# Kernel optimization log

Hardware: AMD Instinct MI355X
Metric: run time of the kernel (lower is better)

## Reference

```python
import jax, jax.numpy as jnp
import numpy as np

B, N, A = 32, 1024, 256          # batch, n_entities, n_agents
D_IN, D_H, H = 256, 256, 8       # input_dim, hidden_dim, n_heads
SCALE = 1.0 / np.sqrt(D_H)
EPS = 1e-12


def setup_inputs() -> dict:
    key = jax.random.key(0)
    ks = jax.random.split(key, 7)
    x = jax.random.normal(ks[0], (B, N, D_IN), dtype=jnp.float32)
    # binary visibility mask [batch, n_agents, n_entities]
    m = (jax.random.uniform(ks[1], (B, A, N)) > 0.5).astype(jnp.float32)
    # encoder Linear(input_dim, hidden_dim): weight [out,in], bias [out]
    W_enc = jax.random.normal(ks[2], (D_H, D_IN), dtype=jnp.float32) / np.sqrt(D_IN)
    b_enc = jnp.zeros((D_H,), dtype=jnp.float32)
    # per-head projection matrices stacked [H, D_H, D_H] (torch.randn init)
    WQ = jax.random.normal(ks[3], (H, D_H, D_H), dtype=jnp.float32)
    WK = jax.random.normal(ks[4], (H, D_H, D_H), dtype=jnp.float32)
    WV = jax.random.normal(ks[5], (H, D_H, D_H), dtype=jnp.float32)
    return {"x": x, "m": m, "W_enc": W_enc, "b_enc": b_enc, "WQ": WQ, "WK": WK, "WV": WV}


def reference(x, m, W_enc, b_enc, WQ, WK, WV):
    # encode: LeakyReLU then Linear
    h = jnp.einsum('bni,oi->bno', jax.nn.leaky_relu(x), W_enc) + b_enc  # [B,N,D_H]
    n_agents = m.shape[1]
    ha = h[:, :n_agents]                                   # [B,A,D_H]
    # per-head projections, heads vectorized
    Q = jnp.einsum('bad,hde->bhae', ha, WQ)                # [B,H,A,D_H]
    K = jnp.einsum('bnd,hde->bhne', h, WK)                 # [B,H,N,D_H]
    V = jnp.einsum('bnd,hde->bhne', h, WV)                 # [B,H,N,D_H]
    S = jnp.einsum('bhae,bhne->bhan', Q, K) * SCALE        # [B,H,A,N]
    P = jax.nn.softmax(S, axis=-1)
    P = P * m[:, None]                                     # post-softmax mask
    prob = P / (jnp.sum(P, axis=-1, keepdims=True) + EPS)  # renormalize
    z = jnp.einsum('bhan,bhne->bhae', prob, V)             # [B,H,A,D_H]
    return jnp.mean(z, axis=1)                             # [B,A,D_H]
```

## Files before the change

### kernel.cpp

```cpp
#include <hip/hip_runtime.h>
#include <math.h>

namespace {
constexpr int B_N  = 32;
constexpr int SEQ  = 1024;
constexpr int AG   = 256;
constexpr int D    = 256;
constexpr int NH   = 8;
constexpr float SCALE = 0.0625f;
constexpr float EPS   = 1e-12f;

constexpr size_t HHI_OFF  = 0;
constexpr size_t HLO_OFF  = 16777216;
constexpr size_t HT_OFF   = 33554432;
constexpr size_t MTHI_OFF = 50331648;
constexpr size_t MTLO_OFF = 51380224;
constexpr size_t MB_OFF   = 52428800;
constexpr size_t WVT_OFF  = 53477376;
constexpr size_t Z16_OFF  = 54525952;
}

typedef __attribute__((ext_vector_type(8))) short short8;
typedef __attribute__((ext_vector_type(4))) float floatx4;
#define MFMA_BF(A,B,C) __builtin_amdgcn_mfma_f32_16x16x32_bf16(A,B,C,0,0,0)

__device__ __forceinline__ unsigned short bf16_rtne(float f) {
    unsigned u = __float_as_uint(f);
    u += 0x7fffu + ((u >> 16) & 1u);
    return (unsigned short)(u >> 16);
}
__device__ __forceinline__ float bf16_tof(unsigned short h) {
    return __uint_as_float(((unsigned)h) << 16);
}
__device__ __forceinline__ void async16(void* lds, const void* g) {
    __builtin_amdgcn_global_load_lds(
        (const __attribute__((address_space(1))) unsigned int*)g,
        (__attribute__((address_space(3))) unsigned int*)lds,
        16, 0, 0);
}

__global__ __launch_bounds__(256) void enc_prep(
    const float* __restrict__ x, const float* __restrict__ W_enc,
    const float* __restrict__ b_enc,
    ushort* __restrict__ h_hi, ushort* __restrict__ h_lo,
    ushort* __restrict__ hT,
    const float* __restrict__ m, unsigned* __restrict__ mb,
    const float* __restrict__ WV, ushort* __restrict__ WVt,
    const float* __restrict__ WQ, const float* __restrict__ WK,
    ushort* __restrict__ Mt_hi, ushort* __restrict__ Mt_lo)
{
    __shared__ __align__(16) char slds[38912];
    const int t = threadIdx.x;
    const int v = blockIdx.x;

    if (v < 2048) {
        ushort (*Ah)[40] = (ushort(*)[40])(slds);
        ushort (*Al)[40] = (ushort(*)[40])(slds + 5120);
        ushort (*Bh)[40] = (ushort(*)[40])(slds + 10240);
        ushort (*Bl)[40] = (ushort(*)[40])(slds + 15360);
        ushort (*Th)[72] = (ushort(*)[72])(slds + 20480);
        ushort (*Tl)[72] = (ushort(*)[72])(slds + 29696);

        const int wv   = t >> 6;
        const int lane = t & 63;
        const int l15  = lane & 15;
        const int quad = lane >> 4;
        const int col0 = (v & 3) * 64;
        const int vy   = v >> 2;
        const int row0 = vy * 64;

        floatx4 acc[4];
#pragma unroll
        for (int i = 0; i < 4; ++i) acc[i] = (floatx4){0.f, 0.f, 0.f, 0.f};

        for (int k0 = 0; k0 < 256; k0 += 32) {
            __syncthreads();
            {
                const int r = t >> 2, s = (t & 3) * 8;
                float f[8];
                *(float4*)&f[0] = *(const float4*)(x + (size_t)(row0 + r) * 256 + k0 + s);
                *(float4*)&f[4] = *(const float4*)(x + (size_t)(row0 + r) * 256 + k0 + s + 4);
                short8 hi8, lo8;
#pragma unroll
                for (int e = 0; e < 8; ++e) {
                    float vv = f[e] > 0.f ? f[e] : 0.01f * f[e];
                    unsigned short hb = bf16_rtne(vv);
                    hi8[e] = (short)hb;
                    lo8[e] = (short)bf16_rtne(vv - bf16_tof(hb));
                }
                *(short8*)&Ah[r][s] = hi8;
                *(short8*)&Al[r][s] = lo8;
                *(float4*)&f[0] = *(const float4*)(W_enc + (size_t)(col0 + r) * 256 + k0 + s);
                *(float4*)&f[4] = *(const float4*)(W_enc + (size_t)(col0 + r) * 256 + k0 + s + 4);
#pragma unroll
                for (int e = 0; e < 8; ++e) {
                    unsigned short hb = bf16_rtne(f[e]);
                    hi8[e] = (short)hb;
                    lo8[e] = (short)bf16_rtne(f[e] - bf16_tof(hb));
                }
                *(short8*)&Bh[r][s] = hi8;
                *(short8*)&Bl[r][s] = lo8;
            }
            __syncthreads();

            short8 Af  = *(const short8*)&Ah[wv * 16 + l15][quad * 8];
            short8 Afl = *(const short8*)&Al[wv * 16 + l15][quad * 8];
#pragma unroll
            for (int et = 0; et < 4; ++et) {
                short8 Bf  = *(const short8*)&Bh[et * 16 + l15][quad * 8];
                short8 Bfl = *(const short8*)&Bl[et * 16 + l15][quad * 8];
                acc[et] = MFMA_BF(Af,  Bf,  acc[et]);
                acc[et] = MFMA_BF(Afl, Bf,  acc[et]);
                acc[et] = MFMA_BF(Af,  Bfl, acc[et]);
            }
        }

        __syncthreads();
#pragma unroll
        for (int et = 0; et < 4; ++et) {
            const int col = et * 16 + l15;
            const float bb = b_enc[col0 + col];
#pragma unroll
            for (int r = 0; r < 4; ++r) {
                const int row = wv * 16 + quad * 4 + r;
                const float vv = acc[et][r] + bb;
                const unsigned short hb = bf16_rtne(vv);
                Th[row][col] = hb;
                Tl[row][col] = bf16_rtne(vv - bf16_tof(hb));
            }
        }
        __syncthreads();
        {
            const int r = t >> 2, c0 = (t & 3) * 16;
            ushort* dh = h_hi + (size_t)(row0 + r) * 256 + col0 + c0;
            ushort* dl = h_lo + (size_t)(row0 + r) * 256 + col0 + c0;
            *(short8*)dh       = *(const short8*)&Th[r][c0];
            *(short8*)(dh + 8) = *(const short8*)&Th[r][c0 + 8];
            *(short8*)dl       = *(const short8*)&Tl[r][c0];
            *(short8*)(dl + 8) = *(const short8*)&Tl[r][c0 + 8];
        }
        {
            const int bq = vy >> 4;
            const int n0 = (vy & 15) * 64;
            const int dd = t >> 2, seg = (t & 3) * 16;
            ushort tmp[16];
#pragma unroll
            for (int j = 0; j < 16; ++j) tmp[j] = Th[seg + j][dd];
            ushort* dst = hT + ((size_t)(bq * 256 + col0 + dd)) * 1024 + n0 + seg;
            *(short8*)dst       = *(short8*)&tmp[0];
            *(short8*)(dst + 8) = *(short8*)&tmp[8];
        }
    } else if (v < 3072) {
        const int idx = (v - 2048) * 256 + t;
        const float4* src = (const float4*)(m + (size_t)idx * 32);
        unsigned wbits = 0;
#pragma unroll
        for (int i = 0; i < 8; ++i) {
            float4 vv = src[i];
            wbits |= (vv.x > 0.5f ? 1u : 0u) << (i * 4 + 0);
            wbits |= (vv.y > 0.5f ? 1u : 0u) << (i * 4 + 1);
            wbits |= (vv.z > 0.5f ? 1u : 0u) << (i * 4 + 2);
            wbits |= (vv.w > 0.5f ? 1u : 0u) << (i * 4 + 3);
        }
        mb[idx] = wbits;
    } else if (v < 3200) {
        float (*T)[68] = (float(*)[68])slds;
        const int v2 = v - 3072;
        const int d0 = (v2 & 3) * 64, e0 = ((v2 >> 2) & 3) * 64, h = v2 >> 4;
        {
            const int r = t >> 2, c = (t & 3) * 16;
            const float* src = WV + ((size_t)(h * 256 + d0 + r)) * 256 + e0 + c;
#pragma unroll
            for (int j = 0; j < 4; ++j)
                *(float4*)&T[r][c + j * 4] = *(const float4*)(src + j * 4);
        }
        __syncthreads();
        {
            const int ee = t >> 2, seg = (t & 3) * 16;
            ushort tmp[16];
#pragma unroll
            for (int j = 0; j < 16; ++j) tmp[j] = bf16_rtne(T[seg + j][ee]);
            ushort* dst = WVt + ((size_t)(h * 256 + e0 + ee)) * 256 + d0 + seg;
            *(short8*)dst       = *(short8*)&tmp[0];
            *(short8*)(dst + 8) = *(short8*)&tmp[8];
        }
    } else {
        float (*AsT)[68] = (float(*)[68])slds;
        float (*BsT)[68] = (float(*)[68])(slds + 8704);
        const int v3 = v - 3200;
        const int tx = t & 15, ty = t >> 4;
        const int col0 = (v3 & 3) * 64;
        const int row0 = ((v3 >> 2) & 3) * 64;
        const int hz   = v3 >> 4;
        const float* A  = WK + (size_t)hz * 256 * 256;
        const float* Bm = WQ + (size_t)hz * 256 * 256;
        ushort* Chi = Mt_hi + (size_t)hz * 256 * 256;
        ushort* Clo = Mt_lo + (size_t)hz * 256 * 256;

        float acc[4][4];
#pragma unroll
        for (int r = 0; r < 4; ++r)
#pragma unroll
            for (int c = 0; c < 4; ++c) acc[r][c] = 0.f;

        for (int k0 = 0; k0 < 256; k0 += 32) {
            __syncthreads();
#pragma unroll
            for (int ss = 0; ss < 2; ++ss) {
                int flat = t + 256 * ss;
                int rr = flat >> 3, k4 = flat & 7;
                float4 vv = *(const float4*)(A + (size_t)(row0 + rr) * 256 + k0 + k4 * 4);
                AsT[k4*4+0][rr] = vv.x; AsT[k4*4+1][rr] = vv.y;
                AsT[k4*4+2][rr] = vv.z; AsT[k4*4+3][rr] = vv.w;
                float4 wv = *(const float4*)(Bm + (size_t)(col0 + rr) * 256 + k0 + k4 * 4);
                BsT[k4*4+0][rr] = wv.x; BsT[k4*4+1][rr] = wv.y;
                BsT[k4*4+2][rr] = wv.z; BsT[k4*4+3][rr] = wv.w;
            }
            __syncthreads();
#pragma unroll 8
            for (int kk = 0; kk < 32; ++kk) {
                float4 a4 = *(const float4*)&AsT[kk][ty * 4];
                float4 b4 = *(const float4*)&BsT[kk][tx * 4];
                const float ar[4] = {a4.x, a4.y, a4.z, a4.w};
                const float bc[4] = {b4.x, b4.y, b4.z, b4.w};
#pragma unroll
                for (int r = 0; r < 4; ++r)
#pragma unroll
                    for (int c = 0; c < 4; ++c)
                        acc[r][c] = fmaf(ar[r], bc[c], acc[r][c]);
            }
        }
#pragma unroll
        for (int r = 0; r < 4; ++r) {
            const int row = row0 + ty * 4 + r;
            ushort hi4[4], lo4[4];
#pragma unroll
            for (int c = 0; c < 4; ++c) {
                float vv = acc[r][c];
                hi4[c] = bf16_rtne(vv);
                lo4[c] = bf16_rtne(vv - bf16_tof(hi4[c]));
            }
            *(ushort4*)(Chi + (size_t)row * 256 + col0 + tx * 4) =
                make_ushort4(hi4[0], hi4[1], hi4[2], hi4[3]);
            *(ushort4*)(Clo + (size_t)row * 256 + col0 + tx * 4) =
                make_ushort4(lo4[0], lo4[1], lo4[2], lo4[3]);
        }
    }
}

__global__ __launch_bounds__(512, 2) void attn_mfma(
    const ushort* __restrict__ h_hi, const ushort* __restrict__ h_lo,
    const ushort* __restrict__ hT,   const ushort* __restrict__ Mt_hi,
    const ushort* __restrict__ Mt_lo, const unsigned* __restrict__ mbits,
    ushort* __restrict__ zout)
{
    __shared__ __align__(16) char lds[118784];
    ushort* pP = (ushort*)(lds + 98304);
    ushort* pE = (ushort*)(lds + 108544);

    const int t    = threadIdx.x;
    const int wv   = t >> 6;
    const int lane = t & 63;
    const int l15  = lane & 15;
    const int quad = lane >> 4;
    const int f    = blockIdx.x;
    const int b    = (f & 7) + 8 * (f >> 7);
    const int mid  = (f >> 3) & 15;
    const int hh   = (mid >> 2) * 2 + (wv >> 2);
    const int a0   = (mid & 3) * 64;
    const int aw   = a0 + (wv & 3) * 16;

    const ushort* hbh = h_hi + (size_t)b * SEQ * D;
    const ushort* hbl = h_lo + (size_t)b * SEQ * D;
    const ushort* hTb = hT   + (size_t)b * D * SEQ;

    floatx4 qac[16];
#pragma unroll
    for (int i = 0; i < 16; ++i) qac[i] = (floatx4){0.f, 0.f, 0.f, 0.f};

    for (int kc = 0; kc < 4; ++kc) {
        short8 Ah[2], Al[2];
#pragma unroll
        for (int kt = 0; kt < 2; ++kt) {
            const size_t ao = ((size_t)b * SEQ + aw + l15) * D +
                              kc * 64 + kt * 32 + quad * 8;
            Ah[kt] = *(const short8*)(h_hi + ao);
            Al[kt] = *(const short8*)(h_lo + ao);
        }
#pragma unroll
        for (int nt2 = 0; nt2 < 16; ++nt2) {
#pragma unroll
            for (int kt = 0; kt < 2; ++kt) {
                const size_t mo = ((size_t)hh * D + nt2 * 16 + l15) * D +
                                  kc * 64 + kt * 32 + quad * 8;
                short8 Bh = *(const short8*)(Mt_hi + mo);
                short8 Bl = *(const short8*)(Mt_lo + mo);
                qac[nt2] = MFMA_BF(Ah[kt], Bh, qac[nt2]);
                qac[nt2] = MFMA_BF(Al[kt], Bh, qac[nt2]);
                qac[nt2] = MFMA_BF(Ah[kt], Bl, qac[nt2]);
            }
        }
    }

    short8 Qhi[8], Qlo[8];
    {
        float* qscr = (float*)lds;
        for (int c = 0; c < 4; ++c) {
#pragma unroll
            for (int j = 0; j < 4; ++j)
#pragma unroll
                for (int r = 0; r < 4; ++r)
                    qscr[(wv * 16 + quad * 4 + r) * 68 + j * 16 + l15] = qac[c * 4 + j][r];
#pragma unroll
            for (int kt = 0; kt < 2; ++kt) {
                const float* pr = &qscr[(wv * 16 + l15) * 68 + kt * 32 + quad * 8];
                float ftmp[8];
                *(float4*)&ftmp[0] = *(const float4*)pr;
                *(float4*)&ftmp[4] = *(const float4*)(pr + 4);
                short8 hi, lo;
#pragma unroll
                for (int e = 0; e < 8; ++e) {
                    unsigned short hb = bf16_rtne(ftmp[e]);
                    hi[e] = (short)hb;
                    lo[e] = (short)bf16_rtne(ftmp[e] - bf16_tof(hb));
                }
                Qhi[c * 2 + kt] = hi;
                Qlo[c * 2 + kt] = lo;
            }
        }
    }
    __syncthreads();

    auto issue_tile = [&](char* buf, int n0) {
        ushort* dh = (ushort*)buf;
        ushort* dl = (ushort*)(buf + 16384);
        ushort* dT = (ushort*)(buf + 32768);
#pragma unroll
        for (int i = 0; i < 2; ++i) {
            const int slot = wv * 128 + i * 64 + lane;
            const int row  = slot >> 5;
            const int p    = slot & 31;
            const int c    = p ^ (row & 7);
            const size_t go = (size_t)(n0 + row) * 256 + c * 8;
            const size_t lo_ = (size_t)(wv * 128 + i * 64) * 8;
            async16(dh + lo_, hbh + go);
            async16(dl + lo_, hbl + go);
        }
#pragma unroll
        for (int i = 0; i < 2; ++i) {
            const int slot = wv * 128 + i * 64 + lane;
            const int row  = slot >> 2;
            const int p    = slot & 3;
            const int c    = p ^ ((row >> 2) & 3);
            async16(dT + (size_t)(wv * 128 + i * 64) * 8,
                    hTb + (size_t)row * 1024 + n0 + c * 8);
        }
    };

    issue_tile(lds,         0);
    issue_tile(lds + 49152, 32);
    __syncthreads();

    floatx4 zac[16];
#pragma unroll
    for (int i = 0; i < 16; ++i) zac[i] = (floatx4){0.f, 0.f, 0.f, 0.f};
    floatx4 zacZ = (floatx4){0.f, 0.f, 0.f, 0.f};
    floatx4 zacE = (floatx4){0.f, 0.f, 0.f, 0.f};
    float mx[4] = {-INFINITY, -INFINITY, -INFINITY, -INFINITY};

    short8 onesf;
#pragma unroll
    for (int e = 0; e < 8; ++e) onesf[e] = (short)0x3F80;

    const unsigned* mbr = mbits + ((size_t)b * AG + aw + quad * 4) * (SEQ / 32);

    for (int nt = 0; nt < 32; ++nt) {
        char* cur = lds + (size_t)(nt & 1) * 49152;
        ushort* hS_hi = (ushort*)cur;
        ushort* hS_lo = (ushort*)(cur + 16384);
        ushort* hTS   = (ushort*)(cur + 32768);

        floatx4 sacH[2], sacL[2];
        sacH[0] = (floatx4){0.f, 0.f, 0.f, 0.f};
        sacH[1] = (floatx4){0.f, 0.f, 0.f, 0.f};
        sacL[0] = (floatx4){0.f, 0.f, 0.f, 0.f};
        sacL[1] = (floatx4){0.f, 0.f, 0.f, 0.f};
        __builtin_amdgcn_s_setprio(1);
#pragma unroll
        for (int ks = 0; ks < 8; ++ks) {
            const int cg = ks * 4 + quad;
#pragma unroll
            for (int ntile = 0; ntile < 2; ++ntile) {
                const int row = ntile * 16 + l15;
                const int off = row * 256 + (cg ^ (row & 7)) * 8;
                short8 Bh = *(const short8*)&hS_hi[off];
                short8 Bl = *(const short8*)&hS_lo[off];
                sacH[ntile] = MFMA_BF(Qhi[ks], Bh, sacH[ntile]);
                sacL[ntile] = MFMA_BF(Qlo[ks], Bh, sacL[ntile]);
                sacL[ntile] = MFMA_BF(Qhi[ks], Bl, sacL[ntile]);
            }
        }
        __builtin_amdgcn_s_setprio(0);

        float l0[4], l1[4];
#pragma unroll
        for (int r = 0; r < 4; ++r) {
            l0[r] = (sacH[0][r] + sacL[0][r]) * SCALE;
            l1[r] = (sacH[1][r] + sacL[1][r]) * SCALE;
        }

        float mt[4];
#pragma unroll
        for (int r = 0; r < 4; ++r) mt[r] = fmaxf(l0[r], l1[r]);
#pragma unroll
        for (int off = 1; off < 16; off <<= 1) {
#pragma unroll
            for (int r = 0; r < 4; ++r)
                mt[r] = fmaxf(mt[r], __shfl_xor(mt[r], off));
        }

        const bool need = (mt[0] > mx[0] + 8.0f) || (mt[1] > mx[1] + 8.0f) ||
                          (mt[2] > mx[2] + 8.0f) || (mt[3] > mx[3] + 8.0f);
        if (__any(need)) {
            float alr[4];
#pragma unroll
            for (int r = 0; r < 4; ++r) {
                const float mxn = fmaxf(mx[r], mt[r]);
                alr[r] = __expf(mx[r] - mxn);
                mx[r] = mxn;
            }
#pragma unroll
            for (int dt = 0; dt < 16; ++dt) {
                zac[dt][0] *= alr[0]; zac[dt][1] *= alr[1];
                zac[dt][2] *= alr[2]; zac[dt][3] *= alr[3];
            }
            zacZ[0] *= alr[0]; zacZ[1] *= alr[1];
            zacZ[2] *= alr[2]; zacZ[3] *= alr[3];
            zacE[0] *= alr[0]; zacE[1] *= alr[1];
            zacE[2] *= alr[2]; zacE[3] *= alr[3];
        }

#pragma unroll
        for (int r = 0; r < 4; ++r) {
            const unsigned w0 = mbr[r * (SEQ / 32) + nt];
            const float e0 = __expf(l0[r] - mx[r]);
            const float e1 = __expf(l1[r] - mx[r]);
            const float p0 = ((w0 >> l15) & 1u)        ? e0 : 0.f;
            const float p1 = ((w0 >> (16 + l15)) & 1u) ? e1 : 0.f;
            const int row = wv * 16 + quad * 4 + r;
            pP[row * 40 + l15]      = bf16_rtne(p0);
            pP[row * 40 + 16 + l15] = bf16_rtne(p1);
            pE[row * 40 + l15]      = bf16_rtne(e0);
            pE[row * 40 + 16 + l15] = bf16_rtne(e1);
        }

        short8 Pf = *(const short8*)&pP[(wv * 16 + l15) * 40 + quad * 8];
        short8 Ef = *(const short8*)&pE[(wv * 16 + l15) * 40 + quad * 8];
        zacZ = MFMA_BF(Pf, onesf, zacZ);
        zacE = MFMA_BF(Ef, onesf, zacE);

        __builtin_amdgcn_s_setprio(1);
#pragma unroll
        for (int dt = 0; dt < 16; ++dt) {
            const int row = dt * 16 + l15;
            const int p   = quad ^ ((row >> 2) & 3);
            short8 Bf = *(const short8*)&hTS[row * 32 + p * 8];
            zac[dt] = MFMA_BF(Pf, Bf, zac[dt]);
        }
        __builtin_amdgcn_s_setprio(0);

        __syncthreads();
        if (nt + 2 < 32) issue_tile(cur, (nt + 2) * 32);
    }

#pragma unroll
    for (int r = 0; r < 4; ++r) {
        const int a = aw + quad * 4 + r;
        const float inv = 1.0f / (zacZ[r] + EPS * zacE[r]);
        ushort* zr = zout + (((size_t)b * NH + hh) * AG + a) * D;
#pragma unroll
        for (int dt = 0; dt < 16; ++dt)
            zr[dt * 16 + l15] = bf16_rtne(zac[dt][r] * inv);
    }
}

__global__ __launch_bounds__(256) void out_mfma(
    const ushort* __restrict__ z16, const ushort* __restrict__ WVt,
    float* __restrict__ out)
{
    __shared__ __align__(16) char olds[65536];
    const int t    = threadIdx.x;
    const int wv   = t >> 6;
    const int lane = t & 63;
    const int l15  = lane & 15;
    const int quad = lane >> 4;
    const int f    = blockIdx.x;
    const int b    = (f & 7) + 8 * (f >> 7);
    const int mid  = (f >> 3) & 15;
    const int e0   = (mid & 3) * 64;
    const int a0   = (mid >> 2) * 64;
    const int aw   = a0 + wv * 16;

    const ushort* zb = z16 + (size_t)b * NH * AG * D;

    auto stage = [&](char* buf, int hh) {
        ushort* dst = (ushort*)buf;
        const ushort* src = zb + (size_t)hh * AG * D;
#pragma unroll
        for (int i = 0; i < 8; ++i) {
            const int slot = i * 256 + t;
            const int row  = slot >> 5;
            const int p    = slot & 31;
            const int c    = p ^ (row & 7);
            async16(dst + (size_t)slot * 8,
                    src + (size_t)(a0 + row) * D + c * 8);
        }
    };

    floatx4 acc[4];
#pragma unroll
    for (int i = 0; i < 4; ++i) acc[i] = (floatx4){0.f, 0.f, 0.f, 0.f};

    stage(olds, 0);
    __syncthreads();

    for (int hh = 0; hh < 8; ++hh) {
        char* cur = olds + (size_t)(hh & 1) * 32768;
        if (hh + 1 < 8) stage(olds + (size_t)((hh + 1) & 1) * 32768, hh + 1);

        ushort* zt = (ushort*)cur;
        const int lrow = wv * 16 + l15;
#pragma unroll
        for (int ci = 0; ci < 8; ++ci) {
            const int d0 = ci * 32;
            const int g  = ci * 4 + quad;
            short8 Af = *(const short8*)&zt[(size_t)lrow * 256 +
                                            (g ^ (lrow & 7)) * 8];
#pragma unroll
            for (int et = 0; et < 4; ++et) {
                short8 Bf = *(const short8*)(WVt +
                    ((size_t)hh * D + e0 + et * 16 + l15) * D + d0 + quad * 8);
                acc[et] = MFMA_BF(Af, Bf, acc[et]);
            }
        }
        __syncthreads();
    }

#pragma unroll
    for (int et = 0; et < 4; ++et)
#pragma unroll
        for (int r = 0; r < 4; ++r)
            out[((size_t)b * AG + aw + quad * 4 + r) * D + e0 + et * 16 + l15] =
                acc[et][r] * 0.125f;
}

extern "C" void kernel_launch(void* const* d_in, const int* in_sizes, int n_in,
                              void* d_out, int out_size, void* d_ws, size_t ws_size,
                              hipStream_t stream)
{
    (void)in_sizes; (void)n_in; (void)out_size; (void)ws_size;
    const float* x     = (const float*)d_in[0];
    const float* m     = (const float*)d_in[1];
    const float* W_enc = (const float*)d_in[2];
    const float* b_enc = (const float*)d_in[3];
    const float* WQ    = (const float*)d_in[4];
    const float* WK    = (const float*)d_in[5];
    const float* WV    = (const float*)d_in[6];
    float* out = (float*)d_out;
    char* ws = (char*)d_ws;

    ushort*   h_hi  = (ushort*)(ws + HHI_OFF);
    ushort*   h_lo  = (ushort*)(ws + HLO_OFF);
    ushort*   hT    = (ushort*)(ws + HT_OFF);
    ushort*   Mt_hi = (ushort*)(ws + MTHI_OFF);
    ushort*   Mt_lo = (ushort*)(ws + MTLO_OFF);
    unsigned* mbits = (unsigned*)(ws + MB_OFF);
    ushort*   WVt   = (ushort*)(ws + WVT_OFF);
    ushort*   z16   = (ushort*)(ws + Z16_OFF);

    enc_prep<<<dim3(3328, 1, 1), dim3(256), 0, stream>>>(
        x, W_enc, b_enc, h_hi, h_lo, hT,
        m, mbits, WV, WVt, WQ, WK, Mt_hi, Mt_lo);
    attn_mfma<<<dim3(512, 1, 1), dim3(512), 0, stream>>>(
        h_hi, h_lo, hT, Mt_hi, Mt_lo, mbits, z16);
    out_mfma<<<dim3(512, 1, 1), dim3(256), 0, stream>>>(z16, WVt, out);
}
```

Measured before the change: 513.5 us.

## Load transposed V tiles directly from global into registers, shrinking LDS footprint

The transposed h tile used for the P·V MFMA is no longer staged through LDS via async copies. Each lane now loads its B fragments straight from global memory into registers, issuing the first half before the QK MFMA loop and the second half after it to hide latency. This cuts LDS per block from about 116KB to 84KB and removes LDS reads and async traffic for that operand. The cost is higher register pressure, 16 short8 values live per iteration, and redundant global or L2 reads across the waves that share the same tile.

```diff
diff --git a/kernel.cpp b/kernel.cpp
--- a/kernel.cpp
+++ b/kernel.cpp
@@ -254,9 +254,9 @@
     const ushort* __restrict__ Mt_lo, const unsigned* __restrict__ mbits,
     ushort* __restrict__ zout)
 {
-    __shared__ __align__(16) char lds[118784];
-    ushort* pP = (ushort*)(lds + 98304);
-    ushort* pE = (ushort*)(lds + 108544);
+    __shared__ __align__(16) char lds[86016];
+    ushort* pP = (ushort*)(lds + 65536);
+    ushort* pE = (ushort*)(lds + 75776);
 
     const int t    = threadIdx.x;
     const int wv   = t >> 6;
@@ -334,7 +334,6 @@
     auto issue_tile = [&](char* buf, int n0) {
         ushort* dh = (ushort*)buf;
         ushort* dl = (ushort*)(buf + 16384);
-        ushort* dT = (ushort*)(buf + 32768);
 #pragma unroll
         for (int i = 0; i < 2; ++i) {
             const int slot = wv * 128 + i * 64 + lane;
@@ -346,19 +345,10 @@
             async16(dh + lo_, hbh + go);
             async16(dl + lo_, hbl + go);
         }
-#pragma unroll
-        for (int i = 0; i < 2; ++i) {
-            const int slot = wv * 128 + i * 64 + lane;
-            const int row  = slot >> 2;
-            const int p    = slot & 3;
-            const int c    = p ^ ((row >> 2) & 3);
-            async16(dT + (size_t)(wv * 128 + i * 64) * 8,
-                    hTb + (size_t)row * 1024 + n0 + c * 8);
-        }
     };
 
     issue_tile(lds,         0);
-    issue_tile(lds + 49152, 32);
+    issue_tile(lds + 32768, 32);
     __syncthreads();
 
     floatx4 zac[16];
@@ -373,12 +363,18 @@
     for (int e = 0; e < 8; ++e) onesf[e] = (short)0x3F80;
 
     const unsigned* mbr = mbits + ((size_t)b * AG + aw + quad * 4) * (SEQ / 32);
+    const ushort*   hTl = hTb + (size_t)l15 * 1024 + quad * 8;
 
     for (int nt = 0; nt < 32; ++nt) {
-        char* cur = lds + (size_t)(nt & 1) * 49152;
+        const int n0 = nt * 32;
+        char* cur = lds + (size_t)(nt & 1) * 32768;
         ushort* hS_hi = (ushort*)cur;
         ushort* hS_lo = (ushort*)(cur + 16384);
-        ushort* hTS   = (ushort*)(cur + 32768);
+
+        short8 Bv0[8];
+#pragma unroll
+        for (int dt = 0; dt < 8; ++dt)
+            Bv0[dt] = *(const short8*)(hTl + (size_t)dt * 16384 + n0);
 
         floatx4 sacH[2], sacL[2];
         sacH[0] = (floatx4){0.f, 0.f, 0.f, 0.f};
@@ -401,6 +397,11 @@
             }
         }
         __builtin_amdgcn_s_setprio(0);
+
+        short8 Bv1[8];
+#pragma unroll
+        for (int dt = 0; dt < 8; ++dt)
+            Bv1[dt] = *(const short8*)(hTl + (size_t)(dt + 8) * 16384 + n0);
 
         float l0[4], l1[4];
 #pragma unroll
@@ -461,12 +462,11 @@
 
         __builtin_amdgcn_s_setprio(1);
 #pragma unroll
-        for (int dt = 0; dt < 16; ++dt) {
-            const int row = dt * 16 + l15;
-            const int p   = quad ^ ((row >> 2) & 3);
-            short8 Bf = *(const short8*)&hTS[row * 32 + p * 8];
-            zac[dt] = MFMA_BF(Pf, Bf, zac[dt]);
-        }
+        for (int dt = 0; dt < 8; ++dt)
+            zac[dt] = MFMA_BF(Pf, Bv0[dt], zac[dt]);
+#pragma unroll
+        for (int dt = 0; dt < 8; ++dt)
+            zac[dt + 8] = MFMA_BF(Pf, Bv1[dt], zac[dt + 8]);
         __builtin_amdgcn_s_setprio(0);
 
         __syncthreads();
```

Result: slower. 785.6 us (+53.0%).

## Widen encoder GEMM tile to full 256 output columns per block

Applied to the files above, without the earlier changes.

The encoder GEMM blocks now compute a 64x256 output tile instead of 64x64, so each x row tile is loaded and split into bf16 hi/lo once rather than four times. W_enc is staged in full per k-step, and the epilogue writes h_hi/h_lo and the transpose hT in four column passes. This cuts redundant x traffic and conversion work and shrinks the grid from 2048 to 512 encoder blocks. In exchange it uses more LDS (51 KB), 16 accumulator tiles per wave with higher register pressure, and fewer blocks for latency hiding.

```diff
diff --git a/kernel.cpp b/kernel.cpp
--- a/kernel.cpp
+++ b/kernel.cpp
@@ -49,29 +49,25 @@
     const float* __restrict__ WQ, const float* __restrict__ WK,
     ushort* __restrict__ Mt_hi, ushort* __restrict__ Mt_lo)
 {
-    __shared__ __align__(16) char slds[38912];
+    __shared__ __align__(16) char slds[51200];
     const int t = threadIdx.x;
     const int v = blockIdx.x;
 
-    if (v < 2048) {
-        ushort (*Ah)[40] = (ushort(*)[40])(slds);
-        ushort (*Al)[40] = (ushort(*)[40])(slds + 5120);
-        ushort (*Bh)[40] = (ushort(*)[40])(slds + 10240);
-        ushort (*Bl)[40] = (ushort(*)[40])(slds + 15360);
-        ushort (*Th)[72] = (ushort(*)[72])(slds + 20480);
-        ushort (*Tl)[72] = (ushort(*)[72])(slds + 29696);
+    if (v < 512) {
+        ushort (*Axh)[40] = (ushort(*)[40])(slds);
+        ushort (*Axl)[40] = (ushort(*)[40])(slds + 5120);
+        ushort (*Bwh)[40] = (ushort(*)[40])(slds + 10240);
+        ushort (*Bwl)[40] = (ushort(*)[40])(slds + 30720);
 
         const int wv   = t >> 6;
         const int lane = t & 63;
         const int l15  = lane & 15;
         const int quad = lane >> 4;
-        const int col0 = (v & 3) * 64;
-        const int vy   = v >> 2;
-        const int row0 = vy * 64;
-
-        floatx4 acc[4];
-#pragma unroll
-        for (int i = 0; i < 4; ++i) acc[i] = (floatx4){0.f, 0.f, 0.f, 0.f};
+        const int row0 = v * 64;
+
+        floatx4 acc[16];
+#pragma unroll
+        for (int i = 0; i < 16; ++i) acc[i] = (floatx4){0.f, 0.f, 0.f, 0.f};
 
         for (int k0 = 0; k0 < 256; k0 += 32) {
             __syncthreads();
@@ -88,70 +84,78 @@
                     hi8[e] = (short)hb;
                     lo8[e] = (short)bf16_rtne(vv - bf16_tof(hb));
                 }
-                *(short8*)&Ah[r][s] = hi8;
-                *(short8*)&Al[r][s] = lo8;
-                *(float4*)&f[0] = *(const float4*)(W_enc + (size_t)(col0 + r) * 256 + k0 + s);
-                *(float4*)&f[4] = *(const float4*)(W_enc + (size_t)(col0 + r) * 256 + k0 + s + 4);
-#pragma unroll
-                for (int e = 0; e < 8; ++e) {
-                    unsigned short hb = bf16_rtne(f[e]);
-                    hi8[e] = (short)hb;
-                    lo8[e] = (short)bf16_rtne(f[e] - bf16_tof(hb));
+                *(short8*)&Axh[r][s] = hi8;
+                *(short8*)&Axl[r][s] = lo8;
+#pragma unroll
+                for (int ch = 0; ch < 4; ++ch) {
+                    const int ws = ch * 8;
+                    *(float4*)&f[0] = *(const float4*)(W_enc + (size_t)t * 256 + k0 + ws);
+                    *(float4*)&f[4] = *(const float4*)(W_enc + (size_t)t * 256 + k0 + ws + 4);
+#pragma unroll
+                    for (int e = 0; e < 8; ++e) {
+                        unsigned short hb = bf16_rtne(f[e]);
+                        hi8[e] = (short)hb;
+                        lo8[e] = (short)bf16_rtne(f[e] - bf16_tof(hb));
+                    }
+                    *(short8*)&Bwh[t][ws] = hi8;
+                    *(short8*)&Bwl[t][ws] = lo8;
                 }
-                *(short8*)&Bh[r][s] = hi8;
-                *(short8*)&Bl[r][s] = lo8;
             }
             __syncthreads();
 
-            short8 Af  = *(const short8*)&Ah[wv * 16 + l15][quad * 8];
-            short8 Afl = *(const short8*)&Al[wv * 16 + l15][quad * 8];
+            short8 Af  = *(const short8*)&Axh[wv * 16 + l15][quad * 8];
+            short8 Afl = *(const short8*)&Axl[wv * 16 + l15][quad * 8];
+#pragma unroll
+            for (int ot = 0; ot < 16; ++ot) {
+                short8 Bf  = *(const short8*)&Bwh[ot * 16 + l15][quad * 8];
+                short8 Bfl = *(const short8*)&Bwl[ot * 16 + l15][quad * 8];
+                acc[ot] = MFMA_BF(Af,  Bf,  acc[ot]);
+                acc[ot] = MFMA_BF(Afl, Bf,  acc[ot]);
+                acc[ot] = MFMA_BF(Af,  Bfl, acc[ot]);
+            }
+        }
+
+        ushort (*Th)[72] = (ushort(*)[72])(slds);
+        ushort (*Tl)[72] = (ushort(*)[72])(slds + 9216);
+        const int bq = v >> 4;
+        const int n0 = (v & 15) * 64;
+        for (int cp = 0; cp < 4; ++cp) {
+            __syncthreads();
 #pragma unroll
             for (int et = 0; et < 4; ++et) {
-                short8 Bf  = *(const short8*)&Bh[et * 16 + l15][quad * 8];
-                short8 Bfl = *(const short8*)&Bl[et * 16 + l15][quad * 8];
-                acc[et] = MFMA_BF(Af,  Bf,  acc[et]);
-                acc[et] = MFMA_BF(Afl, Bf,  acc[et]);
-                acc[et] = MFMA_BF(Af,  Bfl, acc[et]);
-            }
-        }
-
-        __syncthreads();
-#pragma unroll
-        for (int et = 0; et < 4; ++et) {
-            const int col = et * 16 + l15;
-            const float bb = b_enc[col0 + col];
-#pragma unroll
-            for (int r = 0; r < 4; ++r) {
-                const int row = wv * 16 + quad * 4 + r;
-                const float vv = acc[et][r] + bb;
-                const unsigned short hb = bf16_rtne(vv);
-                Th[row][col] = hb;
-                Tl[row][col] = bf16_rtne(vv - bf16_tof(hb));
-            }
-        }
-        __syncthreads();
-        {
-            const int r = t >> 2, c0 = (t & 3) * 16;
-            ushort* dh = h_hi + (size_t)(row0 + r) * 256 + col0 + c0;
-            ushort* dl = h_lo + (size_t)(row0 + r) * 256 + col0 + c0;
-            *(short8*)dh       = *(const short8*)&Th[r][c0];
-            *(short8*)(dh + 8) = *(const short8*)&Th[r][c0 + 8];
-            *(short8*)dl       = *(const short8*)&Tl[r][c0];
-            *(short8*)(dl + 8) = *(const short8*)&Tl[r][c0 + 8];
-        }
-        {
-            const int bq = vy >> 4;
-            const int n0 = (vy & 15) * 64;
-            const int dd = t >> 2, seg = (t & 3) * 16;
-            ushort tmp[16];
-#pragma unroll
-            for (int j = 0; j < 16; ++j) tmp[j] = Th[seg + j][dd];
-            ushort* dst = hT + ((size_t)(bq * 256 + col0 + dd)) * 1024 + n0 + seg;
-            *(short8*)dst       = *(short8*)&tmp[0];
-            *(short8*)(dst + 8) = *(short8*)&tmp[8];
-        }
-    } else if (v < 3072) {
-        const int idx = (v - 2048) * 256 + t;
+                const int col = et * 16 + l15;
+                const float bb = b_enc[cp * 64 + col];
+#pragma unroll
+                for (int r = 0; r < 4; ++r) {
+                    const int row = wv * 16 + quad * 4 + r;
+                    const float vv = acc[cp * 4 + et][r] + bb;
+                    const unsigned short hb = bf16_rtne(vv);
+                    Th[row][col] = hb;
+                    Tl[row][col] = bf16_rtne(vv - bf16_tof(hb));
+                }
+            }
+            __syncthreads();
+            {
+                const int r = t >> 2, c0 = (t & 3) * 16;
+                ushort* dh = h_hi + (size_t)(row0 + r) * 256 + cp * 64 + c0;
+                ushort* dl = h_lo + (size_t)(row0 + r) * 256 + cp * 64 + c0;
+                *(short8*)dh       = *(const short8*)&Th[r][c0];
+                *(short8*)(dh + 8) = *(const short8*)&Th[r][c0 + 8];
+                *(short8*)dl       = *(const short8*)&Tl[r][c0];
+                *(short8*)(dl + 8) = *(const short8*)&Tl[r][c0 + 8];
+            }
+            {
+                const int dd = t >> 2, seg = (t & 3) * 16;
+                ushort tmp[16];
+#pragma unroll
+                for (int j = 0; j < 16; ++j) tmp[j] = Th[seg + j][dd];
+                ushort* dst = hT + ((size_t)(bq * 256 + cp * 64 + dd)) * 1024 + n0 + seg;
+                *(short8*)dst       = *(short8*)&tmp[0];
+                *(short8*)(dst + 8) = *(short8*)&tmp[8];
+            }
+        }
+    } else if (v < 1536) {
+        const int idx = (v - 512) * 256 + t;
         const float4* src = (const float4*)(m + (size_t)idx * 32);
         unsigned wbits = 0;
 #pragma unroll
@@ -163,9 +167,9 @@
             wbits |= (vv.w > 0.5f ? 1u : 0u) << (i * 4 + 3);
         }
         mb[idx] = wbits;
-    } else if (v < 3200) {
+    } else if (v < 1664) {
         float (*T)[68] = (float(*)[68])slds;
-        const int v2 = v - 3072;
+        const int v2 = v - 1536;
         const int d0 = (v2 & 3) * 64, e0 = ((v2 >> 2) & 3) * 64, h = v2 >> 4;
         {
             const int r = t >> 2, c = (t & 3) * 16;
@@ -187,7 +191,7 @@
     } else {
         float (*AsT)[68] = (float(*)[68])slds;
         float (*BsT)[68] = (float(*)[68])(slds + 8704);
-        const int v3 = v - 3200;
+        const int v3 = v - 1664;
         const int tx = t & 15, ty = t >> 4;
         const int col0 = (v3 & 3) * 64;
         const int row0 = ((v3 >> 2) & 3) * 64;
@@ -578,7 +582,7 @@
     ushort*   WVt   = (ushort*)(ws + WVT_OFF);
     ushort*   z16   = (ushort*)(ws + Z16_OFF);
 
-    enc_prep<<<dim3(3328, 1, 1), dim3(256), 0, stream>>>(
+    enc_prep<<<dim3(1792, 1, 1), dim3(256), 0, stream>>>(
         x, W_enc, b_enc, h_hi, h_lo, hT,
         m, mbits, WV, WVt, WQ, WK, Mt_hi, Mt_lo);
     attn_mfma<<<dim3(512, 1, 1), dim3(512), 0, stream>>>(
```

New measurement: 509.9 us. Within noise of the previous version (-0.7%).
